# Kernel optimization log

Hardware: AMD Instinct MI355X
Metric: run time of the kernel (lower is better)

Reference implementation:

```python
import jax, jax.numpy as jnp
import numpy as np

N_GRAPHS = 32
EPS = 1e-5

def dense(x, w, b):
    return x @ w.T + b

def setup_inputs():
    N, E, H, F, G, TH, L = 50000, 800000, 256, 128, 50, 32, 3
    key = jax.random.key(0)
    ks = iter(jax.random.split(key, 48))
    def nrm(shape, s=0.05):
        return jax.random.normal(next(ks), shape, jnp.float32) * s
    return {
        'z': jax.random.randint(next(ks), (N,), 0, 85),
        'tag': jax.random.randint(next(ks), (N,), 0, 3),
        'rel_pos': jax.random.normal(next(ks), (E, 3), jnp.float32),
        'edge_attr': jax.random.uniform(next(ks), (E, G), jnp.float32),
        'edge_index': jax.random.randint(next(ks), (2, E), 0, N),
        'batch': jnp.sort(jax.random.randint(next(ks), (N,), 0, N_GRAPHS)),
        'lin_e1_w': nrm((F // 2, 3)), 'lin_e1_b': jnp.zeros((F // 2,)),
        'lin_e12_w': nrm((F - F // 2, G)), 'lin_e12_b': jnp.zeros((F - F // 2,)),
        'lin_e2_w': nrm((F, F)), 'lin_e2_b': jnp.zeros((F,)),
        'emb_w': nrm((85, H - TH), 1.0),
        'tag_emb_w': nrm((3, TH), 1.0),
        'lin_w': nrm((H, H)), 'lin_b': jnp.zeros((H,)),
        'lin2_w': nrm((H, H)), 'lin2_b': jnp.zeros((H,)),
        'geom_w': nrm((L, F, F)), 'geom_b': jnp.zeros((L, F)),
        'down_w': nrm((L, F, H)), 'down_b': jnp.zeros((L, F)),
        'up_w': nrm((L, H, F)), 'up_b': jnp.zeros((L, H)),
        'gn_w': jnp.ones((L, F)), 'gn_b': jnp.zeros((L, F)), 'gn_ms': jnp.ones((L, F)),
        'out1_w': nrm((H // 2, H)), 'out1_b': jnp.zeros((H // 2,)),
        'out2_w': nrm((1, H // 2)), 'out2_b': jnp.zeros((1,)),
    }

def reference(z, tag, rel_pos, edge_attr, edge_index, batch,
              lin_e1_w, lin_e1_b, lin_e12_w, lin_e12_b, lin_e2_w, lin_e2_b,
              emb_w, tag_emb_w, lin_w, lin_b, lin2_w, lin2_b,
              geom_w, geom_b, down_w, down_b, up_w, up_b,
              gn_w, gn_b, gn_ms, out1_w, out1_b, out2_w, out2_b):
    act = jax.nn.silu  # swish
    N = z.shape[0]
    src, dst = edge_index[0], edge_index[1]
    # EmbeddingBlock: edge embedding e [E,F], node embedding h [N,H]
    e = act(jnp.concatenate([dense(rel_pos, lin_e1_w, lin_e1_b),
                             dense(edge_attr, lin_e12_w, lin_e12_b)], axis=1))
    e = act(dense(e, lin_e2_w, lin_e2_b))
    h = jnp.concatenate([emb_w[z], tag_emb_w[tag]], axis=1)
    h = act(dense(h, lin_w, lin_b))
    h = act(dense(h, lin2_w, lin2_b))
    # InteractionBlocks (mp_type='updownscale', graph_norm) with residual
    L = geom_w.shape[0]
    for l in range(L):
        e_l = act(dense(e, geom_w[l], geom_b[l]))        # [E,F]
        hd = act(dense(h, down_w[l], down_b[l]))         # [N,F]
        msg = hd[src] * e_l                              # gather * filter
        agg = jax.ops.segment_sum(msg, dst, num_segments=N)  # scatter-add
        # GraphNorm with batch=None (single graph): global mean/var
        mean = jnp.mean(agg, axis=0, keepdims=True)
        cen = agg - mean * gn_ms[l]
        var = jnp.mean(cen * cen, axis=0, keepdims=True)
        gn = gn_w[l] * cen / jnp.sqrt(var + EPS) + gn_b[l]
        h = h + act(dense(act(gn), up_w[l], up_b[l]))
    # OutputBlock: node MLP -> per-graph energy
    h1 = act(dense(h, out1_w, out1_b))
    node_e = dense(h1, out2_w, out2_b)                   # [N,1]
    return jax.ops.segment_sum(node_e, batch, num_segments=N_GRAPHS)
```

## Files before the change

### kernel.cpp

```cpp
#include <hip/hip_runtime.h>
#include <math.h>


#define EPS_GN 1e-5f

typedef __attribute__((ext_vector_type(8))) short bf16x8;
typedef __attribute__((ext_vector_type(4))) float f32x4;

__device__ __forceinline__ float silu_f(float x) {
    float e = __expf(-x);
    return x * __builtin_amdgcn_rcpf(1.0f + e);
}
__device__ __forceinline__ float bf2f(unsigned int u) {
    union { unsigned int i; float f; } c;
    c.i = u << 16;
    return c.f;
}
__device__ __forceinline__ unsigned int f2bf(float x) {
    union { float f; unsigned int i; } c;
    c.f = x;
    unsigned int r = c.i + 0x7fffu + ((c.i >> 16) & 1u);
    return r >> 16;
}

enum { A_BF16 = 0, A_F32 = 1 };
enum { ME_STORE_F32 = 0, ME_STORE_BF16 = 1, ME_PERM_BF16 = 2, ME_RESID = 3 };

template<int K, int AMODE, int EPI, bool PRELW>
__global__ __launch_bounds__(256)
void mgemm(const void* __restrict__ Ap, const unsigned short* __restrict__ Wp,
           const float* __restrict__ bias, float* __restrict__ Cf,
           unsigned short* __restrict__ Cb, int M, int NFTOT,
           const int* __restrict__ perm)
{
    constexpr int KS = K / 32;
    const int tid = threadIdx.x;
    const int lane = tid & 63;
    const int wv = tid >> 6;
    const int l16 = lane & 15;
    const int quad = lane >> 4;
    const int m0 = blockIdx.x * 128 + (wv >> 1) * 64;
    const int n0 = blockIdx.y * 128 + (wv & 1) * 64;

    bf16x8 wpre[PRELW ? (KS * 4) : 1];
    if (PRELW) {
#pragma unroll
        for (int t = 0; t < 4; ++t)
#pragma unroll
            for (int s = 0; s < KS; ++s)
                wpre[t * KS + s] = *(const bf16x8*)(Wp +
                    (size_t)(n0 + 16 * t + l16) * K + s * 32 + quad * 8);
    }

    f32x4 acc[4][4];
#pragma unroll
    for (int i = 0; i < 4; ++i)
#pragma unroll
        for (int j = 0; j < 4; ++j) acc[i][j] = (f32x4){0.f, 0.f, 0.f, 0.f};

    for (int s = 0; s < KS; ++s) {
        bf16x8 af[4];
#pragma unroll
        for (int t = 0; t < 4; ++t) {
            int r = m0 + 16 * t + l16;
            if (r >= M) r = M - 1;
            if (AMODE == A_BF16) {
                af[t] = *(const bf16x8*)((const unsigned short*)Ap +
                                         (size_t)r * K + s * 32 + quad * 8);
            } else {
                const float* ap = (const float*)Ap + (size_t)r * K + s * 32 + quad * 8;
                float4 x0 = *(const float4*)ap;
                float4 x1 = *(const float4*)(ap + 4);
                bf16x8 v;
                v[0] = (short)f2bf(x0.x); v[1] = (short)f2bf(x0.y);
                v[2] = (short)f2bf(x0.z); v[3] = (short)f2bf(x0.w);
                v[4] = (short)f2bf(x1.x); v[5] = (short)f2bf(x1.y);
                v[6] = (short)f2bf(x1.z); v[7] = (short)f2bf(x1.w);
                af[t] = v;
            }
        }
        bf16x8 wf[4];
#pragma unroll
        for (int t = 0; t < 4; ++t) {
            if (PRELW) wf[t] = wpre[t * KS + s];
            else       wf[t] = *(const bf16x8*)(Wp +
                           (size_t)(n0 + 16 * t + l16) * K + s * 32 + quad * 8);
        }
#pragma unroll
        for (int tm = 0; tm < 4; ++tm)
#pragma unroll
            for (int tn = 0; tn < 4; ++tn)
                acc[tm][tn] = __builtin_amdgcn_mfma_f32_16x16x32_bf16(
                    wf[tn], af[tm], acc[tm][tn], 0, 0, 0);
    }

    if constexpr (EPI == ME_STORE_BF16 || EPI == ME_PERM_BF16) {
        __shared__ unsigned short sOut[128 * 128];
        const int mwl = (wv >> 1) * 64;
        const int nwl = (wv & 1) * 64;
        const int key = (l16 >> 2) & 3;
#pragma unroll
        for (int tn = 0; tn < 4; ++tn) {
            int cb = nwl + 16 * tn + quad * 4;
            float4 bv = *(const float4*)(bias + cb);
            int cs = cb ^ (key << 4);
#pragma unroll
            for (int tm = 0; tm < 4; ++tm) {
                int r = mwl + 16 * tm + l16;
                ushort4 pk;
                pk.x = (unsigned short)f2bf(silu_f(acc[tm][tn][0] + bv.x));
                pk.y = (unsigned short)f2bf(silu_f(acc[tm][tn][1] + bv.y));
                pk.z = (unsigned short)f2bf(silu_f(acc[tm][tn][2] + bv.z));
                pk.w = (unsigned short)f2bf(silu_f(acc[tm][tn][3] + bv.w));
                *(ushort4*)(sOut + r * 128 + cs) = pk;
            }
        }
        __syncthreads();
#pragma unroll
        for (int rr = 0; rr < 8; ++rr) {
            int r = (wv << 5) + (rr << 2) + quad;
            int gr = blockIdx.x * 128 + r;
            if (gr >= M) continue;
            int cs = (l16 * 8) ^ (((r >> 2) & 3) << 4);
            bf16x8 v = *(const bf16x8*)(sOut + r * 128 + cs);
            int dr = (EPI == ME_PERM_BF16) ? perm[gr] : gr;
            *(bf16x8*)(Cb + (size_t)dr * 128 + l16 * 8) = v;
        }
    } else {
#pragma unroll
        for (int tn = 0; tn < 4; ++tn) {
            int cb = n0 + 16 * tn + quad * 4;
            float4 bv = *(const float4*)(bias + cb);
#pragma unroll
            for (int tm = 0; tm < 4; ++tm) {
                int r = m0 + 16 * tm + l16;
                if (r >= M) continue;
                float4 v;
                v.x = silu_f(acc[tm][tn][0] + bv.x);
                v.y = silu_f(acc[tm][tn][1] + bv.y);
                v.z = silu_f(acc[tm][tn][2] + bv.z);
                v.w = silu_f(acc[tm][tn][3] + bv.w);
                float* dst = Cf + (size_t)r * NFTOT + cb;
                if (EPI == ME_STORE_F32) {
                    *(float4*)dst = v;
                } else {
                    float4 o = *(const float4*)dst;
                    o.x += v.x; o.y += v.y; o.z += v.z; o.w += v.w;
                    *(float4*)dst = o;
                }
            }
        }
    }
}

__global__ __launch_bounds__(256)
void build_wcat(const float* __restrict__ w1, const float* __restrict__ w12,
                const float* __restrict__ b1, const float* __restrict__ b12,
                unsigned short* __restrict__ wcat, float* __restrict__ bcat)
{
    int i = blockIdx.x * 256 + threadIdx.x;
    if (i < 8192) {
        int r = i >> 6, c = i & 63;
        float v = 0.f;
        if (r < 64) { if (c < 3) v = w1[r * 3 + c]; }
        else        { if (c >= 3 && c < 53) v = w12[(r - 64) * 50 + (c - 3)]; }
        wcat[i] = (unsigned short)f2bf(v);
    }
    if (i < 128) bcat[i] = (i < 64) ? b1[i] : b12[i - 64];
}

__global__ __launch_bounds__(256)
void build_eapad(const float* __restrict__ rp, const float* __restrict__ ea,
                 unsigned short* __restrict__ out, int E)
{
    int g = blockIdx.x * 256 + threadIdx.x;
    if (g >= E * 8) return;
    int e = g >> 3, sub = g & 7;
    bf16x8 v;
#pragma unroll
    for (int j = 0; j < 8; ++j) {
        int c = sub * 8 + j;
        float x = 0.f;
        if (c < 3)       x = rp[(size_t)e * 3 + c];
        else if (c < 53) x = ea[(size_t)e * 50 + (c - 3)];
        v[j] = (short)f2bf(x);
    }
    *(bf16x8*)(out + (size_t)g * 8) = v;
}

__global__ __launch_bounds__(256)
void edge_embed_fused(const unsigned short* __restrict__ eapad,
                      const unsigned short* __restrict__ wcat,
                      const float* __restrict__ bcat,
                      const unsigned short* __restrict__ w2,
                      const float* __restrict__ b2,
                      const int* __restrict__ perm,
                      unsigned short* __restrict__ ebf, int E)
{
    __shared__ unsigned short sT[128 * 128];
    const int tid = threadIdx.x;
    const int m0 = blockIdx.x * 128;

    const int lane = tid & 63;
    const int wv = tid >> 6;
    const int l16 = lane & 15, quad = lane >> 4;
    const int mw = (wv >> 1) * 64;
    const int nw = (wv & 1) * 64;

    f32x4 acc[4][4];
#pragma unroll
    for (int i = 0; i < 4; ++i)
#pragma unroll
        for (int j = 0; j < 4; ++j) acc[i][j] = (f32x4){0.f, 0.f, 0.f, 0.f};
#pragma unroll
    for (int s = 0; s < 2; ++s) {
        bf16x8 af[4], wf[4];
#pragma unroll
        for (int t = 0; t < 4; ++t) {
            int r = m0 + mw + 16 * t + l16;
            if (r >= E) r = E - 1;
            af[t] = *(const bf16x8*)(eapad + (size_t)r * 64 + s * 32 + quad * 8);
        }
#pragma unroll
        for (int t = 0; t < 4; ++t)
            wf[t] = *(const bf16x8*)(wcat +
                (size_t)(nw + 16 * t + l16) * 64 + s * 32 + quad * 8);
#pragma unroll
        for (int tm = 0; tm < 4; ++tm)
#pragma unroll
            for (int tn = 0; tn < 4; ++tn)
                acc[tm][tn] = __builtin_amdgcn_mfma_f32_16x16x32_bf16(
                    wf[tn], af[tm], acc[tm][tn], 0, 0, 0);
    }

#pragma unroll
    for (int tn = 0; tn < 4; ++tn) {
        int cb = nw + 16 * tn + quad * 4;
        float4 bv = *(const float4*)(bcat + cb);
#pragma unroll
        for (int tm = 0; tm < 4; ++tm) {
            int r = mw + 16 * tm + l16;
            int g = ((cb >> 3) + r) & 15;
            ushort4 pk;
            pk.x = (unsigned short)f2bf(silu_f(acc[tm][tn][0] + bv.x));
            pk.y = (unsigned short)f2bf(silu_f(acc[tm][tn][1] + bv.y));
            pk.z = (unsigned short)f2bf(silu_f(acc[tm][tn][2] + bv.z));
            pk.w = (unsigned short)f2bf(silu_f(acc[tm][tn][3] + bv.w));
            *(ushort4*)(sT + r * 128 + g * 8 + (cb & 7)) = pk;
        }
    }
    __syncthreads();

    f32x4 acc2[4][4];
#pragma unroll
    for (int i = 0; i < 4; ++i)
#pragma unroll
        for (int j = 0; j < 4; ++j) acc2[i][j] = (f32x4){0.f, 0.f, 0.f, 0.f};
#pragma unroll
    for (int s = 0; s < 4; ++s) {
        bf16x8 af[4], wf[4];
#pragma unroll
        for (int t = 0; t < 4; ++t) {
            int r = mw + 16 * t + l16;
            int g = (s * 4 + quad + r) & 15;
            af[t] = *(const bf16x8*)(sT + r * 128 + g * 8);
        }
#pragma unroll
        for (int t = 0; t < 4; ++t)
            wf[t] = *(const bf16x8*)(w2 +
                (size_t)(nw + 16 * t + l16) * 128 + s * 32 + quad * 8);
#pragma unroll
        for (int tm = 0; tm < 4; ++tm)
#pragma unroll
            for (int tn = 0; tn < 4; ++tn)
                acc2[tm][tn] = __builtin_amdgcn_mfma_f32_16x16x32_bf16(
                    wf[tn], af[tm], acc2[tm][tn], 0, 0, 0);
    }

    __syncthreads();
#pragma unroll
    for (int tn = 0; tn < 4; ++tn) {
        int cb = nw + 16 * tn + quad * 4;
        float4 bv = *(const float4*)(b2 + cb);
#pragma unroll
        for (int tm = 0; tm < 4; ++tm) {
            int r = mw + 16 * tm + l16;
            int cs = cb ^ (((r >> 2) & 3) << 4);
            ushort4 pk;
            pk.x = (unsigned short)f2bf(silu_f(acc2[tm][tn][0] + bv.x));
            pk.y = (unsigned short)f2bf(silu_f(acc2[tm][tn][1] + bv.y));
            pk.z = (unsigned short)f2bf(silu_f(acc2[tm][tn][2] + bv.z));
            pk.w = (unsigned short)f2bf(silu_f(acc2[tm][tn][3] + bv.w));
            *(ushort4*)(sT + r * 128 + cs) = pk;
        }
    }
    __syncthreads();
#pragma unroll
    for (int rr = 0; rr < 8; ++rr) {
        int r = (wv << 5) + (rr << 2) + quad;
        int gr = m0 + r;
        if (gr >= E) continue;
        int cs = (l16 * 8) ^ (((r >> 2) & 3) << 4);
        bf16x8 v = *(const bf16x8*)(sT + r * 128 + cs);
        *(bf16x8*)(ebf + (size_t)perm[gr] * 128 + l16 * 8) = v;
    }
}

__global__ __launch_bounds__(256)
void node_gather(const int* __restrict__ z, const int* __restrict__ tag,
                 const float* __restrict__ embw, const float* __restrict__ tembw,
                 float* __restrict__ hb0, int N)
{
    int lane = threadIdx.x & 63;
    int n = blockIdx.x * 4 + (threadIdx.x >> 6);
    if (n >= N) return;
    int f = lane * 4;
    float4 v;
    if (f < 224) v = *(const float4*)(embw + (size_t)z[n] * 224 + f);
    else         v = *(const float4*)(tembw + (size_t)tag[n] * 32 + (f - 224));
    *(float4*)(hb0 + (size_t)n * 256 + f) = v;
}

__global__ __launch_bounds__(256)
void cvt_all(const float* __restrict__ le2, const float* __restrict__ geom,
             const float* __restrict__ down, const float* __restrict__ up,
             const float* __restrict__ lin, const float* __restrict__ lin2,
             const float* __restrict__ o1, unsigned short* __restrict__ dst)
{
    int i = blockIdx.x * 256 + threadIdx.x;
    if (i >= 425984) return;
    float v;
    if      (i <  16384) v = le2[i];
    else if (i <  65536) v = geom[i - 16384];
    else if (i < 163840) v = down[i - 65536];
    else if (i < 262144) v = up[i - 163840];
    else if (i < 327680) v = lin[i - 262144];
    else if (i < 393216) v = lin2[i - 327680];
    else                 v = o1[i - 393216];
    dst[i] = (unsigned short)f2bf(v);
}

__global__ __launch_bounds__(256)
void edge_hist(const int* __restrict__ dst, int* __restrict__ cnt, int E)
{
    for (int i = blockIdx.x * 256 + threadIdx.x; i < E; i += gridDim.x * 256)
        atomicAdd(&cnt[dst[i]], 1);
}

__global__ __launch_bounds__(1024)
void scan_excl(int* __restrict__ cnt, int N)
{
    __shared__ int sdata[1024];
    __shared__ int s_carry;
    int tid = threadIdx.x;
    if (tid == 0) s_carry = 0;
    __syncthreads();
    for (int base = 0; base < N; base += 1024) {
        int i = base + tid;
        int v = (i < N) ? cnt[i] : 0;
        sdata[tid] = v;
        __syncthreads();
        for (int off = 1; off < 1024; off <<= 1) {
            int t = (tid >= off) ? sdata[tid - off] : 0;
            __syncthreads();
            sdata[tid] += t;
            __syncthreads();
        }
        int excl = sdata[tid] - v + s_carry;
        if (i < N) cnt[i] = excl;
        int tot = sdata[1023];
        __syncthreads();
        if (tid == 0) s_carry += tot;
        __syncthreads();
    }
}

__global__ __launch_bounds__(256)
void edge_rank(const int* __restrict__ src, const int* __restrict__ dst,
               int* __restrict__ cursor, int* __restrict__ rank,
               int* __restrict__ src_s, int E)
{
    for (int i = blockIdx.x * 256 + threadIdx.x; i < E; i += gridDim.x * 256) {
        int d = dst[i];
        int p = atomicAdd(&cursor[d], 1);
        rank[i] = p;
        src_s[p] = src[i];
    }
}

__global__ __launch_bounds__(256)
void csr_gather(const unsigned int* __restrict__ el2,
                const unsigned int* __restrict__ hd2,
                const int* __restrict__ src_s,
                const int* __restrict__ rowend,
                float* __restrict__ agg, int N)
{
    int lane = threadIdx.x & 63;
    int d = blockIdx.x * 4 + (threadIdx.x >> 6);
    if (d >= N) return;
    int start = (d == 0) ? 0 : rowend[d - 1];
    int end = rowend[d];
    float a0 = 0.f, a1 = 0.f;
    int p = start;
    for (; p + 1 < end; p += 2) {
        int s0 = src_s[p], s1 = src_s[p + 1];
        unsigned int e0 = el2[(size_t)p * 64 + lane];
        unsigned int h0 = hd2[(size_t)s0 * 64 + lane];
        unsigned int e1 = el2[(size_t)(p + 1) * 64 + lane];
        unsigned int h1 = hd2[(size_t)s1 * 64 + lane];
        a0 = fmaf(bf2f(e0 & 0xffffu), bf2f(h0 & 0xffffu), a0);
        a1 = fmaf(bf2f(e0 >> 16),     bf2f(h0 >> 16),     a1);
        a0 = fmaf(bf2f(e1 & 0xffffu), bf2f(h1 & 0xffffu), a0);
        a1 = fmaf(bf2f(e1 >> 16),     bf2f(h1 >> 16),     a1);
    }
    if (p < end) {
        int s0 = src_s[p];
        unsigned int e0 = el2[(size_t)p * 64 + lane];
        unsigned int h0 = hd2[(size_t)s0 * 64 + lane];
        a0 = fmaf(bf2f(e0 & 0xffffu), bf2f(h0 & 0xffffu), a0);
        a1 = fmaf(bf2f(e0 >> 16),     bf2f(h0 >> 16),     a1);
    }
    *(float2*)(agg + (size_t)d * 128 + 2 * lane) = make_float2(a0, a1);
}

__global__ __launch_bounds__(256)
void gn_stats(const float* __restrict__ agg, float* __restrict__ sums, int N)
{
    __shared__ float red[512];
    int f = threadIdx.x & 127;
    int sub = threadIdx.x >> 7;
    float s = 0.f, s2 = 0.f;
    for (int r = blockIdx.x * 2 + sub; r < N; r += gridDim.x * 2) {
        float v = agg[(size_t)r * 128 + f];
        s += v;
        s2 += v * v;
    }
    red[threadIdx.x] = s;
    red[256 + threadIdx.x] = s2;
    __syncthreads();
    if (sub == 0) {
        s = red[f] + red[128 + f];
        s2 = red[256 + f] + red[384 + f];
        atomicAdd(&sums[f], s);
        atomicAdd(&sums[128 + f], s2);
    }
}

__global__ void gn_finalize(const float* __restrict__ sums,
                            const float* __restrict__ gnw, const float* __restrict__ gnb,
                            const float* __restrict__ gnms, float* __restrict__ ab,
                            float invN)
{
    int f = threadIdx.x;
    float mean = sums[f] * invN;
    float ex2 = sums[128 + f] * invN;
    float m2 = mean * gnms[f];
    float var = ex2 - 2.f * m2 * mean + m2 * m2;
    float rstd = 1.0f / sqrtf(var + EPS_GN);
    float a = gnw[f] * rstd;
    ab[f] = a;
    ab[128 + f] = gnb[f] - a * m2;
}

__global__ __launch_bounds__(256)
void gn_apply(const float* __restrict__ agg, const float* __restrict__ ab,
              unsigned int* __restrict__ ga, int n2 )
{
    for (int i = blockIdx.x * 256 + threadIdx.x; i < n2; i += gridDim.x * 256) {
        int f = (i & 63) * 2;
        float2 v = *(const float2*)(agg + (size_t)i * 2);
        float r0 = silu_f(ab[f] * v.x + ab[128 + f]);
        float r1 = silu_f(ab[f + 1] * v.y + ab[129 + f]);
        ga[i] = f2bf(r0) | (f2bf(r1) << 16);
    }
}

__global__ __launch_bounds__(256)
void out_reduce(const float* __restrict__ h1, const float* __restrict__ w2,
                const float* __restrict__ b2, const int* __restrict__ batch,
                float* __restrict__ out, int N)
{
    int lane = threadIdx.x & 63;
    int wid = blockIdx.x * 4 + (threadIdx.x >> 6);
    int nwaves = gridDim.x * 4;
    int chunk = (N + nwaves - 1) / nwaves;
    int r0 = wid * chunk;
    int r1 = r0 + chunk; if (r1 > N) r1 = N;
    if (r0 >= r1) return;
    float wa = w2[lane], wb = w2[64 + lane];
    float bb = b2[0];
    int cur = batch[r0];
    float acc = 0.f;
    int cnt = 0;
    for (int r = r0; r < r1; ++r) {
        int g = batch[r];
        if (g != cur) {
            float v = acc;
#pragma unroll
            for (int o = 32; o > 0; o >>= 1) v += __shfl_down(v, o);
            if (lane == 0) atomicAdd(&out[cur], v + (float)cnt * bb);
            cur = g; acc = 0.f; cnt = 0;
        }
        acc = fmaf(h1[(size_t)r * 128 + lane], wa, acc);
        acc = fmaf(h1[(size_t)r * 128 + 64 + lane], wb, acc);
        ++cnt;
    }
    float v = acc;
#pragma unroll
    for (int o = 32; o > 0; o >>= 1) v += __shfl_down(v, o);
    if (lane == 0) atomicAdd(&out[cur], v + (float)cnt * bb);
}

extern "C" void kernel_launch(void* const* d_in, const int* in_sizes, int n_in,
                              void* d_out, int out_size, void* d_ws, size_t ws_size,
                              hipStream_t stream)
{
    const int*   z         = (const int*)d_in[0];
    const int*   tag       = (const int*)d_in[1];
    const float* rel_pos   = (const float*)d_in[2];
    const float* edge_attr = (const float*)d_in[3];
    const int*   eidx      = (const int*)d_in[4];
    const int*   batch     = (const int*)d_in[5];
    const float* le1w  = (const float*)d_in[6];
    const float* le1b  = (const float*)d_in[7];
    const float* le12w = (const float*)d_in[8];
    const float* le12b = (const float*)d_in[9];
    const float* le2w  = (const float*)d_in[10];
    const float* le2b  = (const float*)d_in[11];
    const float* embw  = (const float*)d_in[12];
    const float* tembw = (const float*)d_in[13];
    const float* linw  = (const float*)d_in[14];
    const float* linb  = (const float*)d_in[15];
    const float* lin2w = (const float*)d_in[16];
    const float* lin2b = (const float*)d_in[17];
    const float* geomw = (const float*)d_in[18];
    const float* geomb = (const float*)d_in[19];
    const float* downw = (const float*)d_in[20];
    const float* downb = (const float*)d_in[21];
    const float* upw   = (const float*)d_in[22];
    const float* upb   = (const float*)d_in[23];
    const float* gnw   = (const float*)d_in[24];
    const float* gnb   = (const float*)d_in[25];
    const float* gnms  = (const float*)d_in[26];
    const float* o1w   = (const float*)d_in[27];
    const float* o1b   = (const float*)d_in[28];
    const float* o2w   = (const float*)d_in[29];
    const float* o2b   = (const float*)d_in[30];

    const int N = in_sizes[0];
    const int E = in_sizes[2] / 3;
    const int* esrc = eidx;
    const int* edst = eidx + E;

    char* ws = (char*)d_ws;
    size_t off = 0;
    unsigned short* T = (unsigned short*)(ws + off); off += (size_t)E * 128 * 2;
    unsigned short* ebf = (unsigned short*)(ws + off); off += (size_t)E * 128 * 2;
    float* h   = (float*)(ws + off); off += (size_t)N * 256 * 4;
    float* agg = (float*)(ws + off); off += (size_t)N * 128 * 4;
    unsigned short* hdb = (unsigned short*)(ws + off); off += (size_t)N * 128 * 2;
    int*   cnt   = (int*)(ws + off); off += (size_t)N * 4;
    int*   src_s = (int*)(ws + off); off += (size_t)E * 4;
    unsigned short* wbuf = (unsigned short*)(ws + off); off += 442368ull * 2;
    float* stats = (float*)(ws + off); off += 256 * 4;
    float* ab    = (float*)(ws + off); off += 256 * 4;
    float* bcat  = (float*)(ws + off); off += 128;

    unsigned short* eapad = T;
    float* hb0 = (float*)T;
    float* t1  = (float*)T + (size_t)N * 256;
    unsigned short* el = T;
    int*   rank = (int*)agg;
    unsigned short* ga = hdb;
    float* h1 = agg;

    unsigned short* wb_le2  = wbuf;
    unsigned short* wb_geom = wbuf + 16384;
    unsigned short* wb_down = wbuf + 65536;
    unsigned short* wb_up   = wbuf + 163840;
    unsigned short* wb_lin  = wbuf + 262144;
    unsigned short* wb_lin2 = wbuf + 327680;
    unsigned short* wb_o1   = wbuf + 393216;
    unsigned short* wb_cat  = wbuf + 425984;

    const int mbE = (E + 127) / 128;
    const int mbN = (N + 127) / 128;
    dim3 blk(256);

    cvt_all<<<dim3(1664), blk, 0, stream>>>(
        le2w, geomw, downw, upw, linw, lin2w, o1w, wbuf);
    build_wcat<<<dim3(32), blk, 0, stream>>>(le1w, le12w, le1b, le12b, wb_cat, bcat);
    build_eapad<<<dim3((E * 8 + 255) / 256), blk, 0, stream>>>(
        rel_pos, edge_attr, eapad, E);

    hipMemsetAsync(cnt, 0, (size_t)N * sizeof(int), stream);
    edge_hist<<<dim3(3125), blk, 0, stream>>>(edst, cnt, E);
    scan_excl<<<dim3(1), dim3(1024), 0, stream>>>(cnt, N);
    edge_rank<<<dim3(3125), blk, 0, stream>>>(esrc, edst, cnt, rank, src_s, E);

    edge_embed_fused<<<dim3(mbE), blk, 0, stream>>>(
        eapad, wb_cat, bcat, wb_le2, le2b, rank, ebf, E);

    node_gather<<<dim3((N + 3) / 4), blk, 0, stream>>>(z, tag, embw, tembw, hb0, N);
    mgemm<256, A_F32, ME_STORE_F32, false><<<dim3(mbN, 2), blk, 0, stream>>>(
        hb0, wb_lin, linb, t1, nullptr, N, 256, nullptr);
    mgemm<256, A_F32, ME_STORE_F32, false><<<dim3(mbN, 2), blk, 0, stream>>>(
        t1, wb_lin2, lin2b, h, nullptr, N, 256, nullptr);

    for (int l = 0; l < 3; ++l) {
        mgemm<256, A_F32, ME_STORE_BF16, false><<<dim3(mbN, 1), blk, 0, stream>>>(
            h, wb_down + (size_t)l * 32768, downb + (size_t)l * 128,
            nullptr, hdb, N, 128, nullptr);
        mgemm<128, A_BF16, ME_STORE_BF16, true><<<dim3(mbE, 1), blk, 0, stream>>>(
            ebf, wb_geom + (size_t)l * 16384, geomb + (size_t)l * 128,
            nullptr, el, E, 128, nullptr);
        csr_gather<<<dim3((N + 3) / 4), blk, 0, stream>>>(
            (const unsigned int*)el, (const unsigned int*)hdb, src_s, cnt, agg, N);
        hipMemsetAsync(stats, 0, 256 * sizeof(float), stream);
        gn_stats<<<dim3(256), blk, 0, stream>>>(agg, stats, N);
        gn_finalize<<<dim3(1), dim3(128), 0, stream>>>(
            stats, gnw + (size_t)l * 128, gnb + (size_t)l * 128,
            gnms + (size_t)l * 128, ab, 1.0f / (float)N);
        gn_apply<<<dim3(512), blk, 0, stream>>>(agg, ab, (unsigned int*)ga, N * 64);
        mgemm<128, A_BF16, ME_RESID, true><<<dim3(mbN, 2), blk, 0, stream>>>(
            ga, wb_up + (size_t)l * 32768, upb + (size_t)l * 256,
            h, nullptr, N, 256, nullptr);
    }

    mgemm<256, A_F32, ME_STORE_F32, false><<<dim3(mbN, 1), blk, 0, stream>>>(
        h, wb_o1, o1b, h1, nullptr, N, 128, nullptr);
    hipMemsetAsync(d_out, 0, 32 * sizeof(float), stream);
    out_reduce<<<dim3(512), blk, 0, stream>>>(h1, o2w, o2b, batch, (float*)d_out, N);
}
```

Baseline: 1.840 ms.

## Fuse geometry GEMM with gather-multiply and segmented atomic scatter-add

Replaces the per-layer geometry GEMM that wrote the edge filter to global memory, plus the CSR gather kernel, with one kernel. The new kernel computes the filter tile in LDS, multiplies it by the gathered source features, and does segmented reductions over dst-sorted edges with atomic adds into agg. This removes the write and re-read of the E×128 bf16 filter tensor each layer. In exchange it adds a memset of agg, float atomics at segment boundaries, a serial 32-edge loop per wave, and a nondeterministic summation order.

Measured after the change: 2.191 ms. +19.0%, slower.

```diff
diff --git a/kernel.cpp b/kernel.cpp
--- a/kernel.cpp
+++ b/kernel.cpp
@@ -154,6 +154,101 @@
 }
 
 __global__ __launch_bounds__(256)
+void msg_agg(const unsigned short* __restrict__ ebf,
+             const unsigned short* __restrict__ gw,
+             const float* __restrict__ gb,
+             const unsigned int* __restrict__ hd2,
+             const int* __restrict__ src_s,
+             const int* __restrict__ dsts,
+             float* __restrict__ agg, int E)
+{
+    __shared__ unsigned short sOut[128 * 128];
+    const int tid = threadIdx.x;
+    const int lane = tid & 63;
+    const int wv = tid >> 6;
+    const int l16 = lane & 15;
+    const int quad = lane >> 4;
+    const int m0 = blockIdx.x * 128;
+    const int mw = (wv >> 1) * 64;
+    const int nw = (wv & 1) * 64;
+
+    bf16x8 wpre[16];
+#pragma unroll
+    for (int t = 0; t < 4; ++t)
+#pragma unroll
+        for (int s = 0; s < 4; ++s)
+            wpre[t * 4 + s] = *(const bf16x8*)(gw +
+                (size_t)(nw + 16 * t + l16) * 128 + s * 32 + quad * 8);
+
+    f32x4 acc[4][4];
+#pragma unroll
+    for (int i = 0; i < 4; ++i)
+#pragma unroll
+        for (int j = 0; j < 4; ++j) acc[i][j] = (f32x4){0.f, 0.f, 0.f, 0.f};
+
+#pragma unroll
+    for (int s = 0; s < 4; ++s) {
+        bf16x8 af[4];
+#pragma unroll
+        for (int t = 0; t < 4; ++t) {
+            int r = m0 + mw + 16 * t + l16;
+            if (r >= E) r = E - 1;
+            af[t] = *(const bf16x8*)(ebf + (size_t)r * 128 + s * 32 + quad * 8);
+        }
+#pragma unroll
+        for (int tm = 0; tm < 4; ++tm)
+#pragma unroll
+            for (int tn = 0; tn < 4; ++tn)
+                acc[tm][tn] = __builtin_amdgcn_mfma_f32_16x16x32_bf16(
+                    wpre[tn * 4 + s], af[tm], acc[tm][tn], 0, 0, 0);
+    }
+
+    const int key = (l16 >> 2) & 3;
+#pragma unroll
+    for (int tn = 0; tn < 4; ++tn) {
+        int cb = nw + 16 * tn + quad * 4;
+        float4 bv = *(const float4*)(gb + cb);
+        int cs = cb ^ (key << 4);
+#pragma unroll
+        for (int tm = 0; tm < 4; ++tm) {
+            int r = mw + 16 * tm + l16;
+            ushort4 pk;
+            pk.x = (unsigned short)f2bf(silu_f(acc[tm][tn][0] + bv.x));
+            pk.y = (unsigned short)f2bf(silu_f(acc[tm][tn][1] + bv.y));
+            pk.z = (unsigned short)f2bf(silu_f(acc[tm][tn][2] + bv.z));
+            pk.w = (unsigned short)f2bf(silu_f(acc[tm][tn][3] + bv.w));
+            *(ushort4*)(sOut + r * 128 + cs) = pk;
+        }
+    }
+    __syncthreads();
+
+    int r0 = wv * 32;
+    float a0 = 0.f, a1 = 0.f;
+    int p0 = m0 + r0;
+    int cur = (p0 < E) ? dsts[p0] : -1;
+    for (int i = 0; i < 32; ++i) {
+        int r = r0 + i;
+        int p = m0 + r;
+        if (p >= E) break;
+        int d = dsts[p];
+        if (d != cur) {
+            atomicAdd(&agg[(size_t)cur * 128 + 2 * lane], a0);
+            atomicAdd(&agg[(size_t)cur * 128 + 2 * lane + 1], a1);
+            cur = d; a0 = 0.f; a1 = 0.f;
+        }
+        int cs = (2 * lane) ^ (((r >> 2) & 3) << 4);
+        unsigned int ev = *(const unsigned int*)(sOut + r * 128 + cs);
+        unsigned int hv = hd2[(size_t)src_s[p] * 64 + lane];
+        a0 = fmaf(bf2f(ev & 0xffffu), bf2f(hv & 0xffffu), a0);
+        a1 = fmaf(bf2f(ev >> 16),     bf2f(hv >> 16),     a1);
+    }
+    if (cur >= 0) {
+        atomicAdd(&agg[(size_t)cur * 128 + 2 * lane], a0);
+        atomicAdd(&agg[(size_t)cur * 128 + 2 * lane + 1], a1);
+    }
+}
+
+__global__ __launch_bounds__(256)
 void build_wcat(const float* __restrict__ w1, const float* __restrict__ w12,
                 const float* __restrict__ b1, const float* __restrict__ b12,
                 unsigned short* __restrict__ wcat, float* __restrict__ bcat)
@@ -378,49 +473,15 @@
 __global__ __launch_bounds__(256)
 void edge_rank(const int* __restrict__ src, const int* __restrict__ dst,
                int* __restrict__ cursor, int* __restrict__ rank,
-               int* __restrict__ src_s, int E)
+               int* __restrict__ src_s, int* __restrict__ dsts, int E)
 {
     for (int i = blockIdx.x * 256 + threadIdx.x; i < E; i += gridDim.x * 256) {
         int d = dst[i];
         int p = atomicAdd(&cursor[d], 1);
         rank[i] = p;
         src_s[p] = src[i];
-    }
-}
-
-__global__ __launch_bounds__(256)
-void csr_gather(const unsigned int* __restrict__ el2,
-                const unsigned int* __restrict__ hd2,
-                const int* __restrict__ src_s,
-                const int* __restrict__ rowend,
-                float* __restrict__ agg, int N)
-{
-    int lane = threadIdx.x & 63;
-    int d = blockIdx.x * 4 + (threadIdx.x >> 6);
-    if (d >= N) return;
-    int start = (d == 0) ? 0 : rowend[d - 1];
-    int end = rowend[d];
-    float a0 = 0.f, a1 = 0.f;
-    int p = start;
-    for (; p + 1 < end; p += 2) {
-        int s0 = src_s[p], s1 = src_s[p + 1];
-        unsigned int e0 = el2[(size_t)p * 64 + lane];
-        unsigned int h0 = hd2[(size_t)s0 * 64 + lane];
-        unsigned int e1 = el2[(size_t)(p + 1) * 64 + lane];
-        unsigned int h1 = hd2[(size_t)s1 * 64 + lane];
-        a0 = fmaf(bf2f(e0 & 0xffffu), bf2f(h0 & 0xffffu), a0);
-        a1 = fmaf(bf2f(e0 >> 16),     bf2f(h0 >> 16),     a1);
-        a0 = fmaf(bf2f(e1 & 0xffffu), bf2f(h1 & 0xffffu), a0);
-        a1 = fmaf(bf2f(e1 >> 16),     bf2f(h1 >> 16),     a1);
-    }
-    if (p < end) {
-        int s0 = src_s[p];
-        unsigned int e0 = el2[(size_t)p * 64 + lane];
-        unsigned int h0 = hd2[(size_t)s0 * 64 + lane];
-        a0 = fmaf(bf2f(e0 & 0xffffu), bf2f(h0 & 0xffffu), a0);
-        a1 = fmaf(bf2f(e0 >> 16),     bf2f(h0 >> 16),     a1);
-    }
-    *(float2*)(agg + (size_t)d * 128 + 2 * lane) = make_float2(a0, a1);
+        dsts[p] = d;
+    }
 }
 
 __global__ __launch_bounds__(256)
@@ -561,6 +622,7 @@
     unsigned short* hdb = (unsigned short*)(ws + off); off += (size_t)N * 128 * 2;
     int*   cnt   = (int*)(ws + off); off += (size_t)N * 4;
     int*   src_s = (int*)(ws + off); off += (size_t)E * 4;
+    int*   dsts  = (int*)(ws + off); off += (size_t)E * 4;
     unsigned short* wbuf = (unsigned short*)(ws + off); off += 442368ull * 2;
     float* stats = (float*)(ws + off); off += 256 * 4;
     float* ab    = (float*)(ws + off); off += 256 * 4;
@@ -569,7 +631,6 @@
     unsigned short* eapad = T;
     float* hb0 = (float*)T;
     float* t1  = (float*)T + (size_t)N * 256;
-    unsigned short* el = T;
     int*   rank = (int*)agg;
     unsigned short* ga = hdb;
     float* h1 = agg;
@@ -596,7 +657,7 @@
     hipMemsetAsync(cnt, 0, (size_t)N * sizeof(int), stream);
     edge_hist<<<dim3(3125), blk, 0, stream>>>(edst, cnt, E);
     scan_excl<<<dim3(1), dim3(1024), 0, stream>>>(cnt, N);
-    edge_rank<<<dim3(3125), blk, 0, stream>>>(esrc, edst, cnt, rank, src_s, E);
+    edge_rank<<<dim3(3125), blk, 0, stream>>>(esrc, edst, cnt, rank, src_s, dsts, E);
 
     edge_embed_fused<<<dim3(mbE), blk, 0, stream>>>(
         eapad, wb_cat, bcat, wb_le2, le2b, rank, ebf, E);
@@ -611,11 +672,10 @@
         mgemm<256, A_F32, ME_STORE_BF16, false><<<dim3(mbN, 1), blk, 0, stream>>>(
             h, wb_down + (size_t)l * 32768, downb + (size_t)l * 128,
             nullptr, hdb, N, 128, nullptr);
-        mgemm<128, A_BF16, ME_STORE_BF16, true><<<dim3(mbE, 1), blk, 0, stream>>>(
+        hipMemsetAsync(agg, 0, (size_t)N * 128 * sizeof(float), stream);
+        msg_agg<<<dim3(mbE), blk, 0, stream>>>(
             ebf, wb_geom + (size_t)l * 16384, geomb + (size_t)l * 128,
-            nullptr, el, E, 128, nullptr);
-        csr_gather<<<dim3((N + 3) / 4), blk, 0, stream>>>(
-            (const unsigned int*)el, (const unsigned int*)hdb, src_s, cnt, agg, N);
+            (const unsigned int*)hdb, src_s, dsts, agg, E);
         hipMemsetAsync(stats, 0, 256 * sizeof(float), stream);
         gn_stats<<<dim3(256), blk, 0, stream>>>(agg, stats, N);
         gn_finalize<<<dim3(1), dim3(128), 0, stream>>>(
```
